# Kernel optimization log

Measured on AMD Instinct MI355X. Metric: run time of the kernel, lower is better.

Reference implementation:

```python
import jax, jax.numpy as jnp
import numpy as np

NUM_BINS = 256
EPS = 1e-8


def setup_inputs() -> dict:
    key = jax.random.key(0)
    k1, k2 = jax.random.split(key)
    x = jax.random.uniform(k1, (4096, 8192), dtype=jnp.float32)
    y = jax.random.uniform(k2, (4096, 8192), dtype=jnp.float32)
    return {"x": x, "y": y}


def reference(x, y):
    # min-max normalize to [0, 1]
    xn = (x - jnp.min(x)) / (jnp.max(x) - jnp.min(x) + EPS)
    yn = (y - jnp.min(y)) / (jnp.max(y) - jnp.min(y) + EPS)
    # bin indices, clamped to [0, NUM_BINS-1] (floor(1.0*N) == N gets clipped)
    x_idx = jnp.clip(jnp.floor(xn * NUM_BINS).astype(jnp.int32), 0, NUM_BINS - 1)
    y_idx = jnp.clip(jnp.floor(yn * NUM_BINS).astype(jnp.int32), 0, NUM_BINS - 1)
    n = x.shape[0] * x.shape[1]
    # joint histogram via scatter-add on flattened (x_idx, y_idx) pairs
    flat = (x_idx * NUM_BINS + y_idx).reshape(-1)
    hist_xy = jnp.zeros((NUM_BINS * NUM_BINS,), jnp.float32).at[flat].add(1.0)
    hist_xy = hist_xy.reshape(NUM_BINS, NUM_BINS)
    p_xy = hist_xy / n
    p_x = jnp.sum(p_xy, axis=1)  # marginal over y
    p_y = jnp.sum(p_xy, axis=0)  # marginal over x
    # MI: sum over cells where p_xy>0 and both marginals>0
    px_py = p_x[:, None] * p_y[None, :]
    valid = (p_xy > 0) & (p_x[:, None] > 0) & (p_y[None, :] > 0)
    safe_pxy = jnp.where(valid, p_xy, 1.0)
    safe_den = jnp.where(valid, px_py, 1.0)
    mi = jnp.sum(jnp.where(valid, p_xy * jnp.log(safe_pxy / safe_den), 0.0))
    # normalized MI
    h_x = -jnp.sum(p_x * jnp.log(p_x + EPS))
    h_y = -jnp.sum(p_y * jnp.log(p_y + EPS))
    mi = mi / (jnp.sqrt(h_x * h_y) + EPS)
    return -mi
```

## Files before the change

kernel.cpp:

```cpp
#include <hip/hip_runtime.h>
#include <stdint.h>
#include <math.h>

#define HIST_BINS   65536
#define HIST_WORDS8 16384
#define NTHR_HIST   1024

__device__ __forceinline__ uint32_t f2key(float f){
    uint32_t u = __float_as_uint(f);
    return (u & 0x80000000u) ? ~u : (u | 0x80000000u);
}
__device__ __forceinline__ float key2f(uint32_t k){
    uint32_t u = (k & 0x80000000u) ? (k ^ 0x80000000u) : ~k;
    return __uint_as_float(u);
}


__global__ void init_mm_kernel(uint32_t* __restrict__ mm){
    mm[0] = 0xFFFFFFFFu;
    mm[1] = 0u;
    mm[2] = 0xFFFFFFFFu;
    mm[3] = 0u;
}

__device__ __forceinline__ void mm4(float4 a, float& mn, float& mx){
    mn = fminf(mn, fminf(fminf(a.x, a.y), fminf(a.z, a.w)));
    mx = fmaxf(mx, fmaxf(fmaxf(a.x, a.y), fmaxf(a.z, a.w)));
}

__global__ void __launch_bounds__(1024)
minmax_kernel(const float4* __restrict__ x, const float4* __restrict__ y,
              uint32_t* __restrict__ mm, int n4, int nblk_per){
    int isy = (blockIdx.x >= (unsigned)nblk_per) ? 1 : 0;
    const float4* __restrict__ src = isy ? y : x;
    int bid = blockIdx.x - isy * nblk_per;
    float mn = INFINITY, mx = -INFINITY;
    int stride = nblk_per * blockDim.x;
    int i = bid * blockDim.x + threadIdx.x;
    for (; i + 7 * stride < n4; i += 8 * stride){
        float4 v0 = src[i];
        float4 v1 = src[i +     stride];
        float4 v2 = src[i + 2 * stride];
        float4 v3 = src[i + 3 * stride];
        float4 v4 = src[i + 4 * stride];
        float4 v5 = src[i + 5 * stride];
        float4 v6 = src[i + 6 * stride];
        float4 v7 = src[i + 7 * stride];
        mm4(v0, mn, mx); mm4(v1, mn, mx); mm4(v2, mn, mx); mm4(v3, mn, mx);
        mm4(v4, mn, mx); mm4(v5, mn, mx); mm4(v6, mn, mx); mm4(v7, mn, mx);
    }
    for (; i < n4; i += stride) mm4(src[i], mn, mx);

    #pragma unroll
    for (int off = 32; off > 0; off >>= 1){
        mn = fminf(mn, __shfl_down(mn, off, 64));
        mx = fmaxf(mx, __shfl_down(mx, off, 64));
    }
    __shared__ float smn[16], smx[16];
    int lane = threadIdx.x & 63, wid = threadIdx.x >> 6;
    if (lane == 0){ smn[wid] = mn; smx[wid] = mx; }
    __syncthreads();
    if (threadIdx.x == 0){
        int nw = blockDim.x >> 6;
        for (int w = 1; w < nw; ++w){
            mn = fminf(mn, smn[w]); mx = fmaxf(mx, smx[w]);
        }
        atomicMin(&mm[isy * 2 + 0], f2key(mn));
        atomicMax(&mm[isy * 2 + 1], f2key(mx));
    }
}

__device__ __forceinline__ void bin_pair(float vx, float vy,
                                         float mnx, float sx, float mny, float sy,
                                         uint32_t* lh){
    int ix = (int)floorf((vx - mnx) * sx);
    int iy = (int)floorf((vy - mny) * sy);
    ix = ix < 0 ? 0 : (ix > 255 ? 255 : ix);
    iy = iy < 0 ? 0 : (iy > 255 ? 255 : iy);
    uint32_t bin = ((uint32_t)ix << 8) | (uint32_t)iy;
    atomicAdd(&lh[bin >> 2], 1u << ((bin & 3u) * 8u));
}

__device__ __forceinline__ void bin4(float4 a, float4 b,
                                     float mnx, float sx, float mny, float sy,
                                     uint32_t* lh){
    bin_pair(a.x, b.x, mnx, sx, mny, sy, lh);
    bin_pair(a.y, b.y, mnx, sx, mny, sy, lh);
    bin_pair(a.z, b.z, mnx, sx, mny, sy, lh);
    bin_pair(a.w, b.w, mnx, sx, mny, sy, lh);
}

__global__ void __launch_bounds__(NTHR_HIST)
hist_kernel(const float4* __restrict__ x, const float4* __restrict__ y,
            const uint32_t* __restrict__ mm, uint32_t* __restrict__ out32,
            int n4, int atomic_flush){
    __shared__ uint32_t lh[HIST_WORDS8];
    for (int w = threadIdx.x; w < HIST_WORDS8; w += blockDim.x) lh[w] = 0u;
    __syncthreads();

    float mnx = key2f(mm[0]);
    float sx  = 256.0f / ((key2f(mm[1]) - mnx) + 1e-8f);
    float mny = key2f(mm[2]);
    float sy  = 256.0f / ((key2f(mm[3]) - mny) + 1e-8f);

    int stride = gridDim.x * blockDim.x;
    int i = blockIdx.x * blockDim.x + threadIdx.x;
    for (; i + 3 * stride < n4; i += 4 * stride){
        float4 a0 = x[i], a1 = x[i + stride], a2 = x[i + 2*stride], a3 = x[i + 3*stride];
        float4 b0 = y[i], b1 = y[i + stride], b2 = y[i + 2*stride], b3 = y[i + 3*stride];
        bin4(a0, b0, mnx, sx, mny, sy, lh);
        bin4(a1, b1, mnx, sx, mny, sy, lh);
        bin4(a2, b2, mnx, sx, mny, sy, lh);
        bin4(a3, b3, mnx, sx, mny, sy, lh);
    }
    for (; i < n4; i += stride){
        float4 a = x[i], b = y[i];
        bin4(a, b, mnx, sx, mny, sy, lh);
    }
    __syncthreads();

    if (!atomic_flush){
        uint32_t* part = out32 + (size_t)blockIdx.x * HIST_WORDS8;
        for (int w = threadIdx.x; w < HIST_WORDS8; w += blockDim.x) part[w] = lh[w];
    } else {
        for (int w = threadIdx.x; w < HIST_WORDS8; w += blockDim.x){
            uint32_t v = lh[w];
            if (v){
                uint32_t c0 = v & 255u, c1 = (v >> 8) & 255u, c2 = (v >> 16) & 255u, c3 = v >> 24;
                if (c0) atomicAdd(&out32[4*w + 0], c0);
                if (c1) atomicAdd(&out32[4*w + 1], c1);
                if (c2) atomicAdd(&out32[4*w + 2], c2);
                if (c3) atomicAdd(&out32[4*w + 3], c3);
            }
        }
    }
}

__global__ void __launch_bounds__(1024)
reduce_kernel(const uint32_t* __restrict__ partials, uint32_t* __restrict__ hist,
              int nparts){
    __shared__ uint32_t sm[64][16][16];
    int t = threadIdx.x;
    int ql = t & 15, g = t >> 4;
    int per = nparts >> 6;
    uint32_t c[16];
    #pragma unroll
    for (int k = 0; k < 16; ++k) c[k] = 0;
    const uint4* base = (const uint4*)partials;
    size_t qoff = (size_t)blockIdx.x * 16 + ql;
    #pragma unroll 8
    for (int j = 0; j < per; ++j){
        uint4 v = base[(size_t)(g * per + j) * (HIST_WORDS8 / 4) + qoff];
        c[ 0] += v.x & 255u; c[ 1] += (v.x >> 8) & 255u; c[ 2] += (v.x >> 16) & 255u; c[ 3] += v.x >> 24;
        c[ 4] += v.y & 255u; c[ 5] += (v.y >> 8) & 255u; c[ 6] += (v.y >> 16) & 255u; c[ 7] += v.y >> 24;
        c[ 8] += v.z & 255u; c[ 9] += (v.z >> 8) & 255u; c[10] += (v.z >> 16) & 255u; c[11] += v.z >> 24;
        c[12] += v.w & 255u; c[13] += (v.w >> 8) & 255u; c[14] += (v.w >> 16) & 255u; c[15] += v.w >> 24;
    }
    #pragma unroll
    for (int k = 0; k < 16; ++k) sm[g][k][ql] = c[k];
    __syncthreads();
    if (t < 256){
        int q2 = t & 15;
        int k  = t >> 4;
        uint32_t s = 0;
        #pragma unroll 8
        for (int gg = 0; gg < 64; ++gg) s += sm[gg][k][q2];
        hist[((size_t)blockIdx.x * 16 + q2) * 16 + k] = s;
    }
}

__device__ double bsum1024(double v, double* red, int t){
    #pragma unroll
    for (int off = 32; off > 0; off >>= 1) v += __shfl_down(v, off, 64);
    __syncthreads();
    if ((t & 63) == 0) red[t >> 6] = v;
    __syncthreads();
    if (t == 0){
        double s = 0.0;
        for (int w = 0; w < 16; ++w) s += red[w];
        v = s;
    }
    return v;
}

__global__ void __launch_bounds__(1024)
finalize_kernel(const uint32_t* __restrict__ hist, float* __restrict__ out, int n){
    __shared__ uint32_t rsum[256];
    __shared__ uint32_t csum4[4][256];
    __shared__ uint32_t csum[256];
    __shared__ double red[16];
    int t = threadIdx.x;

    {
        int r = t >> 2, q = t & 3;
        const uint4* hp = (const uint4*)(hist + r * 256 + q * 64);
        uint32_t s = 0;
        #pragma unroll
        for (int k = 0; k < 16; ++k){
            uint4 v = hp[k];
            s += v.x + v.y + v.z + v.w;
        }
        s += __shfl_down(s, 2, 64);
        s += __shfl_down(s, 1, 64);
        if (q == 0) rsum[r] = s;
    }
    {
        int c = t & 255, g = t >> 8;
        const uint32_t* hp = hist + g * 64 * 256 + c;
        uint32_t s = 0;
        #pragma unroll 8
        for (int r = 0; r < 64; ++r) s += hp[r * 256];
        csum4[g][c] = s;
    }
    __syncthreads();
    if (t < 256) csum[t] = csum4[0][t] + csum4[1][t] + csum4[2][t] + csum4[3][t];
    __syncthreads();

    const double invn = 1.0 / (double)n;
    const double dn = (double)n;

    double mi = 0.0;
    {
        int c = t & 255, rb = t >> 8;
        double cs = (double)csum[c];
        for (int k = 0; k < 64; ++k){
            int r = k * 4 + rb;
            uint32_t cnt = hist[r * 256 + c];
            if (cnt){
                double rs = (double)rsum[r];
                double ratio = ((double)cnt * dn) / (rs * cs);
                mi += (double)cnt * (double)logf((float)ratio);
            }
        }
        mi *= invn;
    }
    double hx = 0.0, hy = 0.0;
    if (t < 256){
        double px = (double)rsum[t] * invn;
        double py = (double)csum[t] * invn;
        hx = px * log(px + 1e-8);
        hy = py * log(py + 1e-8);
    }
    double mi_s = bsum1024(mi, red, t);
    double hx_s = bsum1024(hx, red, t);
    double hy_s = bsum1024(hy, red, t);
    if (t == 0){
        double h_x = -hx_s, h_y = -hy_s;
        double nmi = mi_s / (sqrt(h_x * h_y) + 1e-8);
        out[0] = (float)(-nmi);
    }
}

extern "C" void kernel_launch(void* const* d_in, const int* in_sizes, int n_in,
                              void* d_out, int out_size, void* d_ws, size_t ws_size,
                              hipStream_t stream){
    const float* x = (const float*)d_in[0];
    const float* y = (const float*)d_in[1];
    float* out = (float*)d_out;
    uint32_t* ws = (uint32_t*)d_ws;
    uint32_t* hist = ws;
    uint32_t* mm = ws + HIST_BINS;
    uint32_t* partials = ws + HIST_BINS + 64;

    int n  = in_sizes[0];
    int n4 = n / 4;

    size_t need512 = ((size_t)HIST_BINS + 64 + (size_t)512 * HIST_WORDS8) * 4;
    size_t need256 = ((size_t)HIST_BINS + 64 + (size_t)256 * HIST_WORDS8) * 4;
    int nblk, atomic_flush;
    if (ws_size >= need512)      { nblk = 512; atomic_flush = 0; }
    else if (ws_size >= need256) { nblk = 256; atomic_flush = 0; }
    else                         { nblk = 512; atomic_flush = 1; }

    if (atomic_flush)
        hipMemsetAsync(hist, 0, HIST_BINS * sizeof(uint32_t), stream);
    init_mm_kernel<<<1, 1, 0, stream>>>(mm);
    minmax_kernel<<<512, 1024, 0, stream>>>((const float4*)x, (const float4*)y, mm, n4, 256);
    hist_kernel<<<nblk, NTHR_HIST, 0, stream>>>((const float4*)x, (const float4*)y, mm,
                                                atomic_flush ? hist : partials, n4, atomic_flush);
    if (!atomic_flush)
        reduce_kernel<<<256, 1024, 0, stream>>>(partials, hist, nblk);
    finalize_kernel<<<1, 1024, 0, stream>>>(hist, out, n);
}
```

Before: 367.5 us.

## Use contiguous per-block segments in minmax and histogram kernels; resize minmax launch

Both the minmax and histogram kernels now give each block one contiguous segment of the input, where before they used a grid-stride interleave. This is meant to improve DRAM page and cache locality. The minmax kernel moves to 2048 blocks of 256 threads with hard-coded 256-thread strides and a smaller shared reduction. Launch-bound occupancy hints are added to both kernels, though 1024 threads with 8 blocks per CU is likely unachievable for the histogram kernel and may constrain registers. The minmax kernel now assumes blockDim is 256.

```diff
diff --git a/kernel.cpp b/kernel.cpp
--- a/kernel.cpp
+++ b/kernel.cpp
@@ -28,41 +28,45 @@
     mx = fmaxf(mx, fmaxf(fmaxf(a.x, a.y), fmaxf(a.z, a.w)));
 }
 
-__global__ void __launch_bounds__(1024)
+__global__ void __launch_bounds__(256, 8)
 minmax_kernel(const float4* __restrict__ x, const float4* __restrict__ y,
               uint32_t* __restrict__ mm, int n4, int nblk_per){
     int isy = (blockIdx.x >= (unsigned)nblk_per) ? 1 : 0;
     const float4* __restrict__ src = isy ? y : x;
     int bid = blockIdx.x - isy * nblk_per;
+
+    int seg = (n4 + nblk_per - 1) / nblk_per;
+    int start = bid * seg;
+    int end = start + seg; if (end > n4) end = n4;
+
     float mn = INFINITY, mx = -INFINITY;
-    int stride = nblk_per * blockDim.x;
-    int i = bid * blockDim.x + threadIdx.x;
-    for (; i + 7 * stride < n4; i += 8 * stride){
-        float4 v0 = src[i];
-        float4 v1 = src[i +     stride];
-        float4 v2 = src[i + 2 * stride];
-        float4 v3 = src[i + 3 * stride];
-        float4 v4 = src[i + 4 * stride];
-        float4 v5 = src[i + 5 * stride];
-        float4 v6 = src[i + 6 * stride];
-        float4 v7 = src[i + 7 * stride];
+    int base = start;
+    for (; base + 8 * 256 <= end; base += 8 * 256){
+        int i0 = base + threadIdx.x;
+        float4 v0 = src[i0];
+        float4 v1 = src[i0 +  256];
+        float4 v2 = src[i0 +  512];
+        float4 v3 = src[i0 +  768];
+        float4 v4 = src[i0 + 1024];
+        float4 v5 = src[i0 + 1280];
+        float4 v6 = src[i0 + 1536];
+        float4 v7 = src[i0 + 1792];
         mm4(v0, mn, mx); mm4(v1, mn, mx); mm4(v2, mn, mx); mm4(v3, mn, mx);
         mm4(v4, mn, mx); mm4(v5, mn, mx); mm4(v6, mn, mx); mm4(v7, mn, mx);
     }
-    for (; i < n4; i += stride) mm4(src[i], mn, mx);
+    for (int i = base + threadIdx.x; i < end; i += 256) mm4(src[i], mn, mx);
 
     #pragma unroll
     for (int off = 32; off > 0; off >>= 1){
         mn = fminf(mn, __shfl_down(mn, off, 64));
         mx = fmaxf(mx, __shfl_down(mx, off, 64));
     }
-    __shared__ float smn[16], smx[16];
+    __shared__ float smn[4], smx[4];
     int lane = threadIdx.x & 63, wid = threadIdx.x >> 6;
     if (lane == 0){ smn[wid] = mn; smx[wid] = mx; }
     __syncthreads();
     if (threadIdx.x == 0){
-        int nw = blockDim.x >> 6;
-        for (int w = 1; w < nw; ++w){
+        for (int w = 1; w < 4; ++w){
             mn = fminf(mn, smn[w]); mx = fmaxf(mx, smx[w]);
         }
         atomicMin(&mm[isy * 2 + 0], f2key(mn));
@@ -90,7 +94,7 @@
     bin_pair(a.w, b.w, mnx, sx, mny, sy, lh);
 }
 
-__global__ void __launch_bounds__(NTHR_HIST)
+__global__ void __launch_bounds__(NTHR_HIST, 8)
 hist_kernel(const float4* __restrict__ x, const float4* __restrict__ y,
             const uint32_t* __restrict__ mm, uint32_t* __restrict__ out32,
             int n4, int atomic_flush){
@@ -103,17 +107,21 @@
     float mny = key2f(mm[2]);
     float sy  = 256.0f / ((key2f(mm[3]) - mny) + 1e-8f);
 
-    int stride = gridDim.x * blockDim.x;
-    int i = blockIdx.x * blockDim.x + threadIdx.x;
-    for (; i + 3 * stride < n4; i += 4 * stride){
-        float4 a0 = x[i], a1 = x[i + stride], a2 = x[i + 2*stride], a3 = x[i + 3*stride];
-        float4 b0 = y[i], b1 = y[i + stride], b2 = y[i + 2*stride], b3 = y[i + 3*stride];
+    int seg = (n4 + gridDim.x - 1) / gridDim.x;
+    int start = blockIdx.x * seg;
+    int end = start + seg; if (end > n4) end = n4;
+
+    int base = start;
+    for (; base + 4 * 1024 <= end; base += 4 * 1024){
+        int i0 = base + threadIdx.x;
+        float4 a0 = x[i0], a1 = x[i0 + 1024], a2 = x[i0 + 2048], a3 = x[i0 + 3072];
+        float4 b0 = y[i0], b1 = y[i0 + 1024], b2 = y[i0 + 2048], b3 = y[i0 + 3072];
         bin4(a0, b0, mnx, sx, mny, sy, lh);
         bin4(a1, b1, mnx, sx, mny, sy, lh);
         bin4(a2, b2, mnx, sx, mny, sy, lh);
         bin4(a3, b3, mnx, sx, mny, sy, lh);
     }
-    for (; i < n4; i += stride){
+    for (int i = base + threadIdx.x; i < end; i += 1024){
         float4 a = x[i], b = y[i];
         bin4(a, b, mnx, sx, mny, sy, lh);
     }
@@ -275,7 +283,7 @@
     if (atomic_flush)
         hipMemsetAsync(hist, 0, HIST_BINS * sizeof(uint32_t), stream);
     init_mm_kernel<<<1, 1, 0, stream>>>(mm);
-    minmax_kernel<<<512, 1024, 0, stream>>>((const float4*)x, (const float4*)y, mm, n4, 256);
+    minmax_kernel<<<2048, 256, 0, stream>>>((const float4*)x, (const float4*)y, mm, n4, 1024);
     hist_kernel<<<nblk, NTHR_HIST, 0, stream>>>((const float4*)x, (const float4*)y, mm,
                                                 atomic_flush ? hist : partials, n4, atomic_flush);
     if (!atomic_flush)
```

Measured after the change: 369.8 us. About the same (+0.6%).

## Fuse minmax, histogram, reduce and finalize into one cooperative kernel

Applied to the files above, without the earlier changes.

Replaces the chain of separate kernels with a single cooperative kernel. It computes per-block min/max, synchronises the grid, bins each block's own contiguous segment into a shared-memory histogram, writes partials, then reduces and finalizes after further grid syncs. Each block reads back its own segment for binning, which may improve L2 reuse, and launch gaps are removed. The cost is grid-wide barriers, a cap of 256 blocks, and reliance on cooperative launch support and workspace size.

```diff
diff --git a/kernel.cpp b/kernel.cpp
--- a/kernel.cpp
+++ b/kernel.cpp
@@ -1,10 +1,14 @@
 #include <hip/hip_runtime.h>
+#include <hip/hip_cooperative_groups.h>
 #include <stdint.h>
 #include <math.h>
 
+namespace cg = cooperative_groups;
+
 #define HIST_BINS   65536
 #define HIST_WORDS8 16384
-#define NTHR_HIST   1024
+#define NBLK        256
+#define NTHR        1024
 
 __device__ __forceinline__ uint32_t f2key(float f){
     uint32_t u = __float_as_uint(f);
@@ -15,59 +19,9 @@
     return __uint_as_float(u);
 }
 
-
-__global__ void init_mm_kernel(uint32_t* __restrict__ mm){
-    mm[0] = 0xFFFFFFFFu;
-    mm[1] = 0u;
-    mm[2] = 0xFFFFFFFFu;
-    mm[3] = 0u;
-}
-
 __device__ __forceinline__ void mm4(float4 a, float& mn, float& mx){
     mn = fminf(mn, fminf(fminf(a.x, a.y), fminf(a.z, a.w)));
     mx = fmaxf(mx, fmaxf(fmaxf(a.x, a.y), fmaxf(a.z, a.w)));
-}
-
-__global__ void __launch_bounds__(1024)
-minmax_kernel(const float4* __restrict__ x, const float4* __restrict__ y,
-              uint32_t* __restrict__ mm, int n4, int nblk_per){
-    int isy = (blockIdx.x >= (unsigned)nblk_per) ? 1 : 0;
-    const float4* __restrict__ src = isy ? y : x;
-    int bid = blockIdx.x - isy * nblk_per;
-    float mn = INFINITY, mx = -INFINITY;
-    int stride = nblk_per * blockDim.x;
-    int i = bid * blockDim.x + threadIdx.x;
-    for (; i + 7 * stride < n4; i += 8 * stride){
-        float4 v0 = src[i];
-        float4 v1 = src[i +     stride];
-        float4 v2 = src[i + 2 * stride];
-        float4 v3 = src[i + 3 * stride];
-        float4 v4 = src[i + 4 * stride];
-        float4 v5 = src[i + 5 * stride];
-        float4 v6 = src[i + 6 * stride];
-        float4 v7 = src[i + 7 * stride];
-        mm4(v0, mn, mx); mm4(v1, mn, mx); mm4(v2, mn, mx); mm4(v3, mn, mx);
-        mm4(v4, mn, mx); mm4(v5, mn, mx); mm4(v6, mn, mx); mm4(v7, mn, mx);
-    }
-    for (; i < n4; i += stride) mm4(src[i], mn, mx);
-
-    #pragma unroll
-    for (int off = 32; off > 0; off >>= 1){
-        mn = fminf(mn, __shfl_down(mn, off, 64));
-        mx = fmaxf(mx, __shfl_down(mx, off, 64));
-    }
-    __shared__ float smn[16], smx[16];
-    int lane = threadIdx.x & 63, wid = threadIdx.x >> 6;
-    if (lane == 0){ smn[wid] = mn; smx[wid] = mx; }
-    __syncthreads();
-    if (threadIdx.x == 0){
-        int nw = blockDim.x >> 6;
-        for (int w = 1; w < nw; ++w){
-            mn = fminf(mn, smn[w]); mx = fmaxf(mx, smx[w]);
-        }
-        atomicMin(&mm[isy * 2 + 0], f2key(mn));
-        atomicMax(&mm[isy * 2 + 1], f2key(mx));
-    }
 }
 
 __device__ __forceinline__ void bin_pair(float vx, float vy,
@@ -90,85 +44,6 @@
     bin_pair(a.w, b.w, mnx, sx, mny, sy, lh);
 }
 
-__global__ void __launch_bounds__(NTHR_HIST)
-hist_kernel(const float4* __restrict__ x, const float4* __restrict__ y,
-            const uint32_t* __restrict__ mm, uint32_t* __restrict__ out32,
-            int n4, int atomic_flush){
-    __shared__ uint32_t lh[HIST_WORDS8];
-    for (int w = threadIdx.x; w < HIST_WORDS8; w += blockDim.x) lh[w] = 0u;
-    __syncthreads();
-
-    float mnx = key2f(mm[0]);
-    float sx  = 256.0f / ((key2f(mm[1]) - mnx) + 1e-8f);
-    float mny = key2f(mm[2]);
-    float sy  = 256.0f / ((key2f(mm[3]) - mny) + 1e-8f);
-
-    int stride = gridDim.x * blockDim.x;
-    int i = blockIdx.x * blockDim.x + threadIdx.x;
-    for (; i + 3 * stride < n4; i += 4 * stride){
-        float4 a0 = x[i], a1 = x[i + stride], a2 = x[i + 2*stride], a3 = x[i + 3*stride];
-        float4 b0 = y[i], b1 = y[i + stride], b2 = y[i + 2*stride], b3 = y[i + 3*stride];
-        bin4(a0, b0, mnx, sx, mny, sy, lh);
-        bin4(a1, b1, mnx, sx, mny, sy, lh);
-        bin4(a2, b2, mnx, sx, mny, sy, lh);
-        bin4(a3, b3, mnx, sx, mny, sy, lh);
-    }
-    for (; i < n4; i += stride){
-        float4 a = x[i], b = y[i];
-        bin4(a, b, mnx, sx, mny, sy, lh);
-    }
-    __syncthreads();
-
-    if (!atomic_flush){
-        uint32_t* part = out32 + (size_t)blockIdx.x * HIST_WORDS8;
-        for (int w = threadIdx.x; w < HIST_WORDS8; w += blockDim.x) part[w] = lh[w];
-    } else {
-        for (int w = threadIdx.x; w < HIST_WORDS8; w += blockDim.x){
-            uint32_t v = lh[w];
-            if (v){
-                uint32_t c0 = v & 255u, c1 = (v >> 8) & 255u, c2 = (v >> 16) & 255u, c3 = v >> 24;
-                if (c0) atomicAdd(&out32[4*w + 0], c0);
-                if (c1) atomicAdd(&out32[4*w + 1], c1);
-                if (c2) atomicAdd(&out32[4*w + 2], c2);
-                if (c3) atomicAdd(&out32[4*w + 3], c3);
-            }
-        }
-    }
-}
-
-__global__ void __launch_bounds__(1024)
-reduce_kernel(const uint32_t* __restrict__ partials, uint32_t* __restrict__ hist,
-              int nparts){
-    __shared__ uint32_t sm[64][16][16];
-    int t = threadIdx.x;
-    int ql = t & 15, g = t >> 4;
-    int per = nparts >> 6;
-    uint32_t c[16];
-    #pragma unroll
-    for (int k = 0; k < 16; ++k) c[k] = 0;
-    const uint4* base = (const uint4*)partials;
-    size_t qoff = (size_t)blockIdx.x * 16 + ql;
-    #pragma unroll 8
-    for (int j = 0; j < per; ++j){
-        uint4 v = base[(size_t)(g * per + j) * (HIST_WORDS8 / 4) + qoff];
-        c[ 0] += v.x & 255u; c[ 1] += (v.x >> 8) & 255u; c[ 2] += (v.x >> 16) & 255u; c[ 3] += v.x >> 24;
-        c[ 4] += v.y & 255u; c[ 5] += (v.y >> 8) & 255u; c[ 6] += (v.y >> 16) & 255u; c[ 7] += v.y >> 24;
-        c[ 8] += v.z & 255u; c[ 9] += (v.z >> 8) & 255u; c[10] += (v.z >> 16) & 255u; c[11] += v.z >> 24;
-        c[12] += v.w & 255u; c[13] += (v.w >> 8) & 255u; c[14] += (v.w >> 16) & 255u; c[15] += v.w >> 24;
-    }
-    #pragma unroll
-    for (int k = 0; k < 16; ++k) sm[g][k][ql] = c[k];
-    __syncthreads();
-    if (t < 256){
-        int q2 = t & 15;
-        int k  = t >> 4;
-        uint32_t s = 0;
-        #pragma unroll 8
-        for (int gg = 0; gg < 64; ++gg) s += sm[gg][k][q2];
-        hist[((size_t)blockIdx.x * 16 + q2) * 16 + k] = s;
-    }
-}
-
 __device__ double bsum1024(double v, double* red, int t){
     #pragma unroll
     for (int off = 32; off > 0; off >>= 1) v += __shfl_down(v, off, 64);
@@ -183,14 +58,10 @@
     return v;
 }
 
-__global__ void __launch_bounds__(1024)
-finalize_kernel(const uint32_t* __restrict__ hist, float* __restrict__ out, int n){
-    __shared__ uint32_t rsum[256];
-    __shared__ uint32_t csum4[4][256];
-    __shared__ uint32_t csum[256];
-    __shared__ double red[16];
+__device__ void finalize_dev(const uint32_t* __restrict__ hist, float* __restrict__ out,
+                             int n, uint32_t* rsum, uint32_t* csum4, uint32_t* csum,
+                             double* red){
     int t = threadIdx.x;
-
     {
         int r = t >> 2, q = t & 3;
         const uint4* hp = (const uint4*)(hist + r * 256 + q * 64);
@@ -210,15 +81,14 @@
         uint32_t s = 0;
         #pragma unroll 8
         for (int r = 0; r < 64; ++r) s += hp[r * 256];
-        csum4[g][c] = s;
-    }
-    __syncthreads();
-    if (t < 256) csum[t] = csum4[0][t] + csum4[1][t] + csum4[2][t] + csum4[3][t];
+        csum4[g * 256 + c] = s;
+    }
+    __syncthreads();
+    if (t < 256) csum[t] = csum4[t] + csum4[256 + t] + csum4[512 + t] + csum4[768 + t];
     __syncthreads();
 
     const double invn = 1.0 / (double)n;
     const double dn = (double)n;
-
     double mi = 0.0;
     {
         int c = t & 255, rb = t >> 8;
@@ -251,34 +121,246 @@
     }
 }
 
+__global__ void __launch_bounds__(NTHR, 4)
+fused_kernel(const float4* __restrict__ x, const float4* __restrict__ y,
+             uint32_t* __restrict__ ws, float* __restrict__ out, int n, int n4){
+    union SM {
+        uint32_t lh[HIST_WORDS8];
+        uint32_t sm[64][16][16];
+        struct {
+            uint32_t rsum[256];
+            uint32_t csum4[1024];
+            uint32_t csum[256];
+            double   red[16];
+        } fin;
+    };
+    __shared__ SM s;
+    __shared__ float sxn[16], sxx[16], syn[16], syx[16];
+    __shared__ float scale_sh[4];
+
+    uint32_t* hist     = ws;
+    float*    blockmm  = (float*)(ws + HIST_BINS);
+    uint32_t* partials = ws + HIST_BINS + 1024;
+
+    cg::grid_group grid = cg::this_grid();
+    int t   = threadIdx.x;
+    int bid = blockIdx.x;
+    int seg   = (n4 + NBLK - 1) / NBLK;
+    int start = bid * seg;
+    int end   = start + seg; if (end > n4) end = n4;
+
+    float mnx = INFINITY, mxx = -INFINITY, mny = INFINITY, mxy = -INFINITY;
+    for (int i = start + t; i < end; i += NTHR){
+        float4 a = x[i], b = y[i];
+        mm4(a, mnx, mxx);
+        mm4(b, mny, mxy);
+    }
+    #pragma unroll
+    for (int off = 32; off > 0; off >>= 1){
+        mnx = fminf(mnx, __shfl_down(mnx, off, 64));
+        mxx = fmaxf(mxx, __shfl_down(mxx, off, 64));
+        mny = fminf(mny, __shfl_down(mny, off, 64));
+        mxy = fmaxf(mxy, __shfl_down(mxy, off, 64));
+    }
+    if ((t & 63) == 0){
+        int w = t >> 6;
+        sxn[w] = mnx; sxx[w] = mxx; syn[w] = mny; syx[w] = mxy;
+    }
+    __syncthreads();
+    if (t == 0){
+        for (int w = 1; w < 16; ++w){
+            mnx = fminf(mnx, sxn[w]); mxx = fmaxf(mxx, sxx[w]);
+            mny = fminf(mny, syn[w]); mxy = fmaxf(mxy, syx[w]);
+        }
+        ((float4*)blockmm)[bid] = make_float4(mnx, mxx, mny, mxy);
+    }
+    grid.sync();
+
+    for (int w = t; w < HIST_WORDS8; w += NTHR) s.lh[w] = 0u;
+    if (t < NBLK){
+        float4 m = ((const float4*)blockmm)[t];
+        float a = m.x, b = m.y, c = m.z, d = m.w;
+        #pragma unroll
+        for (int off = 32; off > 0; off >>= 1){
+            a = fminf(a, __shfl_down(a, off, 64));
+            b = fmaxf(b, __shfl_down(b, off, 64));
+            c = fminf(c, __shfl_down(c, off, 64));
+            d = fmaxf(d, __shfl_down(d, off, 64));
+        }
+        if ((t & 63) == 0){
+            int w = t >> 6;
+            sxn[w] = a; sxx[w] = b; syn[w] = c; syx[w] = d;
+        }
+    }
+    __syncthreads();
+    if (t == 0){
+        float a = sxn[0], b = sxx[0], c = syn[0], d = syx[0];
+        for (int w = 1; w < 4; ++w){
+            a = fminf(a, sxn[w]); b = fmaxf(b, sxx[w]);
+            c = fminf(c, syn[w]); d = fmaxf(d, syx[w]);
+        }
+        scale_sh[0] = a;
+        scale_sh[1] = 256.0f / ((b - a) + 1e-8f);
+        scale_sh[2] = c;
+        scale_sh[3] = 256.0f / ((d - c) + 1e-8f);
+    }
+    __syncthreads();
+
+    {
+        float gmnx = scale_sh[0], gsx = scale_sh[1];
+        float gmny = scale_sh[2], gsy = scale_sh[3];
+        int base = start;
+        for (; base + 4 * NTHR <= end; base += 4 * NTHR){
+            int i0 = base + t;
+            float4 a0 = x[i0], a1 = x[i0 + NTHR], a2 = x[i0 + 2*NTHR], a3 = x[i0 + 3*NTHR];
+            float4 b0 = y[i0], b1 = y[i0 + NTHR], b2 = y[i0 + 2*NTHR], b3 = y[i0 + 3*NTHR];
+            bin4(a0, b0, gmnx, gsx, gmny, gsy, s.lh);
+            bin4(a1, b1, gmnx, gsx, gmny, gsy, s.lh);
+            bin4(a2, b2, gmnx, gsx, gmny, gsy, s.lh);
+            bin4(a3, b3, gmnx, gsx, gmny, gsy, s.lh);
+        }
+        for (int i = base + t; i < end; i += NTHR){
+            float4 a = x[i], b = y[i];
+            bin4(a, b, gmnx, gsx, gmny, gsy, s.lh);
+        }
+    }
+    __syncthreads();
+    {
+        uint32_t* part = partials + (size_t)bid * HIST_WORDS8;
+        for (int w = t; w < HIST_WORDS8; w += NTHR) part[w] = s.lh[w];
+    }
+    grid.sync();
+
+    {
+        int ql = t & 15, g = t >> 4;
+        uint32_t c[16];
+        #pragma unroll
+        for (int k = 0; k < 16; ++k) c[k] = 0;
+        const uint4* basep = (const uint4*)partials;
+        size_t qoff = (size_t)bid * 16 + ql;
+        #pragma unroll
+        for (int j = 0; j < 4; ++j){
+            uint4 v = basep[(size_t)(g * 4 + j) * (HIST_WORDS8 / 4) + qoff];
+            c[ 0] += v.x & 255u; c[ 1] += (v.x >> 8) & 255u; c[ 2] += (v.x >> 16) & 255u; c[ 3] += v.x >> 24;
+            c[ 4] += v.y & 255u; c[ 5] += (v.y >> 8) & 255u; c[ 6] += (v.y >> 16) & 255u; c[ 7] += v.y >> 24;
+            c[ 8] += v.z & 255u; c[ 9] += (v.z >> 8) & 255u; c[10] += (v.z >> 16) & 255u; c[11] += v.z >> 24;
+            c[12] += v.w & 255u; c[13] += (v.w >> 8) & 255u; c[14] += (v.w >> 16) & 255u; c[15] += v.w >> 24;
+        }
+        #pragma unroll
+        for (int k = 0; k < 16; ++k) s.sm[g][k][ql] = c[k];
+        __syncthreads();
+        if (t < 256){
+            int q2 = t & 15, k = t >> 4;
+            uint32_t sum = 0;
+            #pragma unroll 8
+            for (int gg = 0; gg < 64; ++gg) sum += s.sm[gg][k][q2];
+            hist[((size_t)bid * 16 + q2) * 16 + k] = sum;
+        }
+    }
+    grid.sync();
+
+    if (bid == 0)
+        finalize_dev(hist, out, n, s.fin.rsum, s.fin.csum4, s.fin.csum, s.fin.red);
+}
+
+__global__ void init_mm_kernel(uint32_t* __restrict__ mm){
+    mm[0] = 0xFFFFFFFFu; mm[1] = 0u; mm[2] = 0xFFFFFFFFu; mm[3] = 0u;
+}
+
+__global__ void __launch_bounds__(1024)
+minmax_legacy(const float4* __restrict__ x, const float4* __restrict__ y,
+              uint32_t* __restrict__ mm, int n4){
+    __shared__ float sxn[16], sxx[16], syn[16], syx[16];
+    float mnx = INFINITY, mxx = -INFINITY, mny = INFINITY, mxy = -INFINITY;
+    int stride = gridDim.x * blockDim.x;
+    for (int i = blockIdx.x * blockDim.x + threadIdx.x; i < n4; i += stride){
+        mm4(x[i], mnx, mxx);
+        mm4(y[i], mny, mxy);
+    }
+    #pragma unroll
+    for (int off = 32; off > 0; off >>= 1){
+        mnx = fminf(mnx, __shfl_down(mnx, off, 64));
+        mxx = fmaxf(mxx, __shfl_down(mxx, off, 64));
+        mny = fminf(mny, __shfl_down(mny, off, 64));
+        mxy = fmaxf(mxy, __shfl_down(mxy, off, 64));
+    }
+    int t = threadIdx.x;
+    if ((t & 63) == 0){
+        int w = t >> 6;
+        sxn[w] = mnx; sxx[w] = mxx; syn[w] = mny; syx[w] = mxy;
+    }
+    __syncthreads();
+    if (t == 0){
+        int nw = blockDim.x >> 6;
+        for (int w = 1; w < nw; ++w){
+            mnx = fminf(mnx, sxn[w]); mxx = fmaxf(mxx, sxx[w]);
+            mny = fminf(mny, syn[w]); mxy = fmaxf(mxy, syx[w]);
+        }
+        atomicMin(&mm[0], f2key(mnx));
+        atomicMax(&mm[1], f2key(mxx));
+        atomicMin(&mm[2], f2key(mny));
+        atomicMax(&mm[3], f2key(mxy));
+    }
+}
+
+__global__ void __launch_bounds__(1024)
+hist_legacy(const float4* __restrict__ x, const float4* __restrict__ y,
+            const uint32_t* __restrict__ mm, uint32_t* __restrict__ hist, int n4){
+    __shared__ uint32_t lh[HIST_WORDS8];
+    for (int w = threadIdx.x; w < HIST_WORDS8; w += blockDim.x) lh[w] = 0u;
+    __syncthreads();
+    float mnx = key2f(mm[0]);
+    float sx  = 256.0f / ((key2f(mm[1]) - mnx) + 1e-8f);
+    float mny = key2f(mm[2]);
+    float sy  = 256.0f / ((key2f(mm[3]) - mny) + 1e-8f);
+    int stride = gridDim.x * blockDim.x;
+    for (int i = blockIdx.x * blockDim.x + threadIdx.x; i < n4; i += stride)
+        bin4(x[i], y[i], mnx, sx, mny, sy, lh);
+    __syncthreads();
+    for (int w = threadIdx.x; w < HIST_WORDS8; w += blockDim.x){
+        uint32_t v = lh[w];
+        if (v){
+            uint32_t c0 = v & 255u, c1 = (v >> 8) & 255u, c2 = (v >> 16) & 255u, c3 = v >> 24;
+            if (c0) atomicAdd(&hist[4*w + 0], c0);
+            if (c1) atomicAdd(&hist[4*w + 1], c1);
+            if (c2) atomicAdd(&hist[4*w + 2], c2);
+            if (c3) atomicAdd(&hist[4*w + 3], c3);
+        }
+    }
+}
+
+__global__ void __launch_bounds__(1024)
+finalize_kernel(const uint32_t* __restrict__ hist, float* __restrict__ out, int n){
+    __shared__ uint32_t rsum[256];
+    __shared__ uint32_t csum4[1024];
+    __shared__ uint32_t csum[256];
+    __shared__ double red[16];
+    finalize_dev(hist, out, n, rsum, csum4, csum, red);
+}
+
 extern "C" void kernel_launch(void* const* d_in, const int* in_sizes, int n_in,
                               void* d_out, int out_size, void* d_ws, size_t ws_size,
                               hipStream_t stream){
-    const float* x = (const float*)d_in[0];
-    const float* y = (const float*)d_in[1];
+    const float4* x = (const float4*)d_in[0];
+    const float4* y = (const float4*)d_in[1];
     float* out = (float*)d_out;
     uint32_t* ws = (uint32_t*)d_ws;
-    uint32_t* hist = ws;
-    uint32_t* mm = ws + HIST_BINS;
-    uint32_t* partials = ws + HIST_BINS + 64;
 
     int n  = in_sizes[0];
     int n4 = n / 4;
 
-    size_t need512 = ((size_t)HIST_BINS + 64 + (size_t)512 * HIST_WORDS8) * 4;
-    size_t need256 = ((size_t)HIST_BINS + 64 + (size_t)256 * HIST_WORDS8) * 4;
-    int nblk, atomic_flush;
-    if (ws_size >= need512)      { nblk = 512; atomic_flush = 0; }
-    else if (ws_size >= need256) { nblk = 256; atomic_flush = 0; }
-    else                         { nblk = 512; atomic_flush = 1; }
-
-    if (atomic_flush)
+    size_t need = ((size_t)HIST_BINS + 1024 + (size_t)NBLK * HIST_WORDS8) * 4;
+    if (ws_size >= need){
+        void* args[] = {(void*)&x, (void*)&y, (void*)&ws, (void*)&out, (void*)&n, (void*)&n4};
+        hipLaunchCooperativeKernel((const void*)fused_kernel, dim3(NBLK), dim3(NTHR),
+                                   args, 0, stream);
+    } else {
+        uint32_t* hist = ws;
+        uint32_t* mm   = ws + HIST_BINS;
         hipMemsetAsync(hist, 0, HIST_BINS * sizeof(uint32_t), stream);
-    init_mm_kernel<<<1, 1, 0, stream>>>(mm);
-    minmax_kernel<<<512, 1024, 0, stream>>>((const float4*)x, (const float4*)y, mm, n4, 256);
-    hist_kernel<<<nblk, NTHR_HIST, 0, stream>>>((const float4*)x, (const float4*)y, mm,
-                                                atomic_flush ? hist : partials, n4, atomic_flush);
-    if (!atomic_flush)
-        reduce_kernel<<<256, 1024, 0, stream>>>(partials, hist, nblk);
-    finalize_kernel<<<1, 1024, 0, stream>>>(hist, out, n);
-}
+        init_mm_kernel<<<1, 1, 0, stream>>>(mm);
+        minmax_legacy<<<512, 1024, 0, stream>>>(x, y, mm, n4);
+        hist_legacy<<<512, 1024, 0, stream>>>(x, y, mm, hist, n4);
+        finalize_kernel<<<1, 1024, 0, stream>>>(hist, out, n);
+    }
+}
```

Result: slower. 451.3 us (+22.8%).
